# Performance work log

Measured on AMD Instinct MI355X. Metric: run time of the kernel, lower is better.

Reference implementation:

```python
import jax, jax.numpy as jnp
import numpy as np

N_NODES = 50000
N_EDGES = 800000
LN_EPS = 1e-5


def _segment_softmax_aggr(msg, t, dst, n):
    # SoftmaxAggregation(learn=True): alpha = softmax(msg * t) per dest segment, out = sum(alpha * msg)
    logits = msg * t  # [E, C]
    m = jax.ops.segment_max(logits, dst, num_segments=n)
    m = jnp.where(jnp.isfinite(m), m, 0.0)  # empty segments -> 0 to keep exp finite
    e = jnp.exp(logits - m[dst])
    denom = jax.ops.segment_sum(e, dst, num_segments=n)
    alpha = e / jnp.maximum(denom[dst], 1e-16)
    return jax.ops.segment_sum(alpha * msg, dst, num_segments=n)


def _sage_conv(x, src, dst, wp, bp, t, wl, bl, wr):
    # project=True: messages come from relu(lin(x)); root term uses ORIGINAL x
    xp = jax.nn.relu(x @ wp + bp)
    msg = xp[src]                                   # [E, C] gather
    aggr = _segment_softmax_aggr(msg, t, dst, x.shape[0])
    out = aggr @ wl + bl + x @ wr
    # normalize=True: L2 normalize rows (eps as in F.normalize)
    nrm = jnp.maximum(jnp.linalg.norm(out, axis=-1, keepdims=True), 1e-12)
    return out / nrm


def _mem_pool(x, k, w_conv, wl, bl):
    # PyG MemPooling, tau=1: Student-t kernel 1/(1+d^2)
    H, K, F = k.shape
    kk = k.reshape(H * K, F)
    d2 = (jnp.sum(kk * kk, -1)[:, None] + jnp.sum(x * x, -1)[None, :]
          - 2.0 * kk @ x.T)                          # [H*K, N]
    d2 = jnp.maximum(d2, 0.0)
    dist = 1.0 / (1.0 + d2)
    dist = dist.reshape(H, K, -1).transpose(0, 2, 1)  # [H, N, K]
    S = dist / jnp.sum(dist, -1, keepdims=True)       # per-head normalize over clusters
    S = jnp.einsum('h,hnk->nk', w_conv, S)            # 1x1 conv mixing heads (no bias)
    S = jax.nn.softmax(S, axis=-1)                    # [N, K]
    xp = S.T @ x                                      # [K, F]
    return xp @ wl + bl                               # [K, out]


def setup_inputs() -> dict:
    key = jax.random.key(0)
    ks = jax.random.split(key, 20)
    rn = lambda i, shp, s: jax.random.normal(ks[i], shp, dtype=jnp.float32) * s
    inp = {
        'x': rn(0, (N_NODES, 64), 1.0),
        'edge_index': jax.random.randint(ks[1], (2, N_EDGES), 0, N_NODES, dtype=jnp.int32),
        'w_proj1': rn(2, (64, 64), 0.1), 'b_proj1': rn(3, (64,), 0.05),
        't1': jnp.ones((64,), jnp.float32),
        'w_l1': rn(4, (64, 256), 0.1), 'b_l1': rn(5, (256,), 0.05),
        'w_r1': rn(6, (64, 256), 0.1),
        'w_proj2': rn(7, (256, 256), 0.05), 'b_proj2': rn(8, (256,), 0.05),
        't2': jnp.ones((256,), jnp.float32),
        'w_l2': rn(9, (256, 128), 0.05), 'b_l2': rn(10, (128,), 0.05),
        'w_r2': rn(11, (256, 128), 0.05),
        'k_mem': rn(12, (4, 4, 128), 1.0),
        'w_conv': rn(13, (4,), 0.5),
        'w_memlin': rn(14, (128, 128), 0.08), 'b_memlin': rn(15, (128,), 0.05),
        'w_fx': rn(16, (128, 64), 0.08), 'b_fx': rn(17, (64,), 0.05),
        'gamma': jnp.ones((64,), jnp.float32),
        'beta': jnp.zeros((64,), jnp.float32),
    }
    return inp


def reference(x, edge_index, w_proj1, b_proj1, t1, w_l1, b_l1, w_r1,
              w_proj2, b_proj2, t2, w_l2, b_l2, w_r2,
              k_mem, w_conv, w_memlin, b_memlin, w_fx, b_fx, gamma, beta):
    src, dst = edge_index[0], edge_index[1]
    h = _sage_conv(x, src, dst, w_proj1, b_proj1, t1, w_l1, b_l1, w_r1)
    h = jax.nn.relu(h)                              # dropout = identity (eval)
    h = _sage_conv(h, src, dst, w_proj2, b_proj2, t2, w_l2, b_l2, w_r2)
    h = jax.nn.relu(h)
    pooled = _mem_pool(h, k_mem, w_conv, w_memlin, b_memlin)  # [4, 128]
    g = jnp.mean(pooled, axis=0, keepdims=True)     # global_mean_pool -> [1, 128]
    y = g @ w_fx + b_fx                             # [1, 64]
    mu = jnp.mean(y, -1, keepdims=True)
    var = jnp.var(y, -1, keepdims=True)
    y = (y - mu) / jnp.sqrt(var + LN_EPS) * gamma + beta
    return jax.nn.relu(y)
```

## Files before the change

kernel.cpp:

```cpp
#include <hip/hip_runtime.h>
#include <hip/hip_bf16.h>

#define N_NODES 50000
#define N_EDGES 800000
#define NB 196
#define NBK 512
#define EPB 1563
#define PC_SLICES 2048
#define NWAVES 8192

typedef __attribute__((ext_vector_type(8))) short short8;
typedef __attribute__((ext_vector_type(4))) float f32x4;
typedef __attribute__((ext_vector_type(2))) float f32x2;

#define QSCALE2 (2.f / 255.f)
#define QINV2   127.5f
#define QSCALE1 (12.75f / 255.f)
#define QINV1   20.f

__device__ __forceinline__ float us2f(unsigned short u) {
    return __uint_as_float(((unsigned int)u) << 16);
}
__device__ __forceinline__ unsigned short f2bu(float f) {
    unsigned int u = __float_as_uint(f);
    unsigned int r = (u + 0x7fffu + ((u >> 16) & 1u)) >> 16;
    return (unsigned short)r;
}
__device__ __forceinline__ float exp2_hw(float x) {
    float r;
    __asm__("v_exp_f32 %0, %1" : "=v"(r) : "v"(x));
    return r;
}
__device__ __forceinline__ void async16(const void* g, void* l) {
    __builtin_amdgcn_global_load_lds(
        (const __attribute__((address_space(1))) unsigned int*)g,
        (__attribute__((address_space(3))) unsigned int*)l, 16, 0, 0);
}
#define LOG2E 1.44269504088896f

__global__ void k_hist(const int* __restrict__ dst, int* __restrict__ counts) {
    int e = blockIdx.x * 256 + threadIdx.x;
    if (e < N_EDGES) atomicAdd(&counts[dst[e]], 1);
}

__global__ __launch_bounds__(256) void k_scan1(const int* __restrict__ counts,
                                               int* __restrict__ row_ptr,
                                               int* __restrict__ partial) {
    __shared__ int sd[256];
    int t = threadIdx.x, i = blockIdx.x * 256 + t;
    int v = (i < N_NODES) ? counts[i] : 0;
    sd[t] = v;
    __syncthreads();
    for (int off = 1; off < 256; off <<= 1) {
        int o = (t >= off) ? sd[t - off] : 0;
        __syncthreads();
        sd[t] += o;
        __syncthreads();
    }
    if (i < N_NODES) row_ptr[i] = sd[t] - v;
    if (t == 255) partial[blockIdx.x] = sd[255];
}

__global__ __launch_bounds__(256) void k_scan3b(int* __restrict__ row_ptr,
                                                const int* __restrict__ partial) {
    __shared__ int sd[256];
    int t = threadIdx.x;
    sd[t] = (t < blockIdx.x) ? partial[t] : 0;
    __syncthreads();
    for (int off = 128; off > 0; off >>= 1) {
        if (t < off) sd[t] += sd[t + off];
        __syncthreads();
    }
    int base = sd[0];
    int i = blockIdx.x * 256 + t;
    if (i < N_NODES) row_ptr[i] += base;
    if (blockIdx.x == 0 && t == 0) row_ptr[N_NODES] = N_EDGES;
}

__global__ __launch_bounds__(256) void k_bhist(const int* __restrict__ dst,
                                               int* __restrict__ bcnt) {
    __shared__ int h[196];
    int t = threadIdx.x, b = blockIdx.x;
    if (t < 196) h[t] = 0;
    __syncthreads();
    int e0 = b * EPB, e1 = e0 + EPB < N_EDGES ? e0 + EPB : N_EDGES;
    for (int e = e0 + t; e < e1; e += 256) atomicAdd(&h[dst[e] >> 8], 1);
    __syncthreads();
    if (t < 196) bcnt[b * 196 + t] = h[t];
}

__global__ __launch_bounds__(512) void k_bscan(const int* __restrict__ bcnt,
                                               const int* __restrict__ row_ptr,
                                               int* __restrict__ boff) {
    __shared__ int sd[512];
    int q = blockIdx.x, t = threadIdx.x;
    int v = bcnt[t * 196 + q];
    sd[t] = v;
    __syncthreads();
    for (int off = 1; off < 512; off <<= 1) {
        int o = (t >= off) ? sd[t - off] : 0;
        __syncthreads();
        sd[t] += o;
        __syncthreads();
    }
    boff[t * 196 + q] = row_ptr[q * 256] + sd[t] - v;
}

__global__ __launch_bounds__(256) void k_bucket2(const int* __restrict__ src,
                                                 const int* __restrict__ dst,
                                                 const int* __restrict__ boff,
                                                 int* __restrict__ tmp) {
    __shared__ int lcur[196];
    int t = threadIdx.x, b = blockIdx.x;
    if (t < 196) lcur[t] = boff[b * 196 + t];
    __syncthreads();
    int e0 = b * EPB, e1 = e0 + EPB < N_EDGES ? e0 + EPB : N_EDGES;
    for (int e = e0 + t; e < e1; e += 256) {
        int d = dst[e];
        int pos = atomicAdd(&lcur[d >> 8], 1);
        tmp[pos] = src[e] | ((d & 255) << 16);
    }
}

__global__ __launch_bounds__(256) void k_scatter2(const int* __restrict__ row_ptr,
                                                  const int* __restrict__ tmp,
                                                  int* __restrict__ src_sorted) {
    __shared__ int lcur[256];
    int b = blockIdx.x, t = threadIdx.x;
    int n0 = b * 256;
    int nhi = n0 + 256 < N_NODES ? n0 + 256 : N_NODES;
    if (n0 + t < nhi) lcur[t] = row_ptr[n0 + t];
    __syncthreads();
    int ebeg = row_ptr[n0], eend = row_ptr[nhi];
    for (int i = ebeg + t; i < eend; i += 256) {
        int w = tmp[i];
        int pos = atomicAdd(&lcur[(w >> 16) & 255], 1);
        src_sorted[pos] = w & 0xFFFF;
    }
}

__global__ __launch_bounds__(256) void k_split(const int* __restrict__ row_ptr,
                                               int* __restrict__ split) {
    int w = blockIdx.x * 256 + threadIdx.x;
    if (w > NWAVES) return;
    if (w == NWAVES) { split[w] = N_NODES; return; }
    int target = (int)((long long)w * N_EDGES / NWAVES);
    int lo = 0, hi = N_NODES;
    while (lo < hi) {
        int mid = (lo + hi) >> 1;
        if (row_ptr[mid] < target) lo = mid + 1; else hi = mid;
    }
    split[w] = lo;
}

#define XCAST_N (N_NODES * 64)
#define PREP_TOT (XCAST_N + 167936)
__global__ __launch_bounds__(256) void k_prep(const float* __restrict__ x,
                                              const float* __restrict__ wp1,
                                              const float* __restrict__ wl1,
                                              const float* __restrict__ wr1,
                                              const float* __restrict__ wp2,
                                              const float* __restrict__ wl2,
                                              const float* __restrict__ wr2,
                                              unsigned short* __restrict__ cat1,
                                              unsigned short* __restrict__ B0T,
                                              unsigned short* __restrict__ B1T,
                                              unsigned short* __restrict__ BP2T,
                                              unsigned short* __restrict__ B2T) {
    int idx = (blockIdx.x * 256 + threadIdx.x) * 4;
    if (idx < XCAST_N) {
        int i = idx >> 6, j = idx & 63;
        float4 v = *(const float4*)&x[idx];
        ushort4 o = { f2bu(v.x), f2bu(v.y), f2bu(v.z), f2bu(v.w) };
        *(ushort4*)&cat1[i * 128 + 64 + j] = o;
        return;
    }
    int w = idx - XCAST_N;
    if (w < 4096)  { float4 v = *(const float4*)&wp1[w]; int k = w >> 6, n = w & 63;
                     B0T[n*64+k]=f2bu(v.x); B0T[(n+1)*64+k]=f2bu(v.y);
                     B0T[(n+2)*64+k]=f2bu(v.z); B0T[(n+3)*64+k]=f2bu(v.w); return; }
    w -= 4096;
    if (w < 16384) { float4 v = *(const float4*)&wl1[w]; int k = w >> 8, n = w & 255;
                     B1T[n*128+k]=f2bu(v.x); B1T[(n+1)*128+k]=f2bu(v.y);
                     B1T[(n+2)*128+k]=f2bu(v.z); B1T[(n+3)*128+k]=f2bu(v.w); return; }
    w -= 16384;
    if (w < 16384) { float4 v = *(const float4*)&wr1[w]; int k = w >> 8, n = w & 255;
                     B1T[n*128+64+k]=f2bu(v.x); B1T[(n+1)*128+64+k]=f2bu(v.y);
                     B1T[(n+2)*128+64+k]=f2bu(v.z); B1T[(n+3)*128+64+k]=f2bu(v.w); return; }
    w -= 16384;
    if (w < 65536) { float4 v = *(const float4*)&wp2[w]; int k = w >> 8, n = w & 255;
                     BP2T[n*256+k]=f2bu(v.x); BP2T[(n+1)*256+k]=f2bu(v.y);
                     BP2T[(n+2)*256+k]=f2bu(v.z); BP2T[(n+3)*256+k]=f2bu(v.w); return; }
    w -= 65536;
    if (w < 32768) { float4 v = *(const float4*)&wl2[w]; int k = w >> 7, n = w & 127;
                     B2T[n*512+k]=f2bu(v.x); B2T[(n+1)*512+k]=f2bu(v.y);
                     B2T[(n+2)*512+k]=f2bu(v.z); B2T[(n+3)*512+k]=f2bu(v.w); return; }
    w -= 32768;
    if (w < 32768) { float4 v = *(const float4*)&wr2[w]; int k = w >> 7, n = w & 127;
                     B2T[n*512+256+k]=f2bu(v.x); B2T[(n+1)*512+256+k]=f2bu(v.y);
                     B2T[(n+2)*512+256+k]=f2bu(v.z); B2T[(n+3)*512+256+k]=f2bu(v.w); return; }
}

template<int K, int C, int LDA, int LDOUT, int OUT_OFF, int EP, int WPB, int MH, int PIPE>
__global__ __launch_bounds__(256, WPB) void k_gemm(const unsigned short* __restrict__ A,
                                                   const unsigned short* __restrict__ BT,
                                                   const float* __restrict__ bias,
                                                   void* __restrict__ outv,
                                                   const float* __restrict__ kmem,
                                                   const float* __restrict__ wconv,
                                                   float* __restrict__ Sm,
                                                   float qinv) {
    constexpr int NT = C / 16;
    constexpr int SAE = 64 * MH * 64;
    constexpr int SBE = C * 64;
    constexpr int BUFE = SAE + SBE;
    constexpr int STAGE_B = BUFE * 2 * (PIPE ? 2 : 1);
    constexpr int RPLD = (EP == 2) ? (C + 4) : ((EP == 3) ? (C + 16) : (C + 8));
    constexpr int RP_B = 64 * RPLD * (EP == 2 ? 4 : (EP == 3 ? 1 : 2));
    constexpr int SMEM_B = STAGE_B > RP_B ? STAGE_B : RP_B;
    constexpr int POOL_B = (EP == 2) ? (2048 * 4 + 64 + 16) : 16;
    __shared__ __align__(16) char smem[SMEM_B + POOL_B];
    unsigned short* sA = (unsigned short*)smem;
    float* kls  = (float*)(smem + SMEM_B);
    float* kk2s = kls + 2048;
    float* wcs  = kk2s + 16;

    int t = threadIdx.x;
    int wid = t >> 6, lane = t & 63;
    int lrow = lane & 15, quad = lane >> 4;
    int m0 = blockIdx.x * (64 * MH);

    if (EP == 2) {
        for (int i = t; i < 2048; i += 256) kls[i] = kmem[i];
        if (t < 4) wcs[t] = wconv[t];
        __syncthreads();
        if (t < 16) {
            float s = 0.f;
            for (int f = 0; f < 128; ++f) { float v = kls[t * 128 + f]; s += v * v; }
            kk2s[t] = s;
        }
    }

    f32x4 acc[MH][NT];
#pragma unroll
    for (int h = 0; h < MH; ++h)
#pragma unroll
        for (int nt = 0; nt < NT; ++nt)
#pragma unroll
            for (int r = 0; r < 4; ++r) acc[h][nt][r] = 0.f;

    auto stage = [&](int step, int buf) {
        unsigned short* sAb = sA + buf * BUFE;
        unsigned short* sBb = sAb + SAE;
        int k0 = step * 64;
        for (int i = t; i < 64 * MH * 8; i += 256) {
            int r = i >> 3, seg = i & 7;
            size_t m = (size_t)(m0 + r);
            async16(&A[m * LDA + k0 + ((seg ^ (r & 7)) << 3)],
                    (char*)sAb + (size_t)(i - lane) * 16);
        }
        for (int i = t; i < C * 8; i += 256) {
            int n = i >> 3, seg = i & 7;
            async16(&BT[(size_t)n * K + k0 + ((seg ^ (n & 7)) << 3)],
                    (char*)sBb + (size_t)(i - lane) * 16);
        }
    };
    auto compute = [&](int buf) {
        unsigned short* sAb = sA + buf * BUFE;
        unsigned short* sBb = sAb + SAE;
#pragma unroll
        for (int kk = 0; kk < 2; ++kk) {
            int sw = lrow & 7;
            short8 av[MH];
#pragma unroll
            for (int h = 0; h < MH; ++h)
                av[h] = *(const short8*)&sAb[(h * 64 + wid * 16 + lrow) * 64 +
                                             (((kk * 4 + quad) ^ sw) << 3)];
#pragma unroll
            for (int nt = 0; nt < NT; ++nt) {
                short8 bfg = *(const short8*)&sBb[(nt * 16 + lrow) * 64 +
                                                  (((kk * 4 + quad) ^ sw) << 3)];
#pragma unroll
                for (int h = 0; h < MH; ++h)
                    acc[h][nt] = __builtin_amdgcn_mfma_f32_16x16x32_bf16(av[h], bfg, acc[h][nt], 0, 0, 0);
            }
        }
    };

    constexpr int NSTEP = K / 64;
    if (PIPE) {
        stage(0, 0);
        __syncthreads();
        for (int step = 0; step < NSTEP; ++step) {
            int cur = step & 1;
            if (step + 1 < NSTEP) stage(step + 1, cur ^ 1);
            compute(cur);
            __syncthreads();
        }
    } else {
        for (int step = 0; step < NSTEP; ++step) {
            __syncthreads();
            stage(step, 0);
            __syncthreads();
            compute(0);
        }
    }

#pragma unroll
    for (int h = 0; h < MH; ++h) {
#pragma unroll
        for (int nt = 0; nt < NT; ++nt) {
            float bv = bias[nt * 16 + lrow];
#pragma unroll
            for (int r = 0; r < 4; ++r) acc[h][nt][r] += bv;
        }
        if (EP == 1 || EP == 2) {
#pragma unroll
            for (int r = 0; r < 4; ++r) {
                float ss = 0.f;
#pragma unroll
                for (int nt = 0; nt < NT; ++nt) ss += acc[h][nt][r] * acc[h][nt][r];
                ss += __shfl_xor(ss, 1);
                ss += __shfl_xor(ss, 2);
                ss += __shfl_xor(ss, 4);
                ss += __shfl_xor(ss, 8);
                float rinv = 1.f / fmaxf(sqrtf(ss), 1e-12f);
#pragma unroll
                for (int nt = 0; nt < NT; ++nt)
                    acc[h][nt][r] = fmaxf(acc[h][nt][r] * rinv, 0.f);
            }
        } else {
#pragma unroll
            for (int nt = 0; nt < NT; ++nt)
#pragma unroll
                for (int r = 0; r < 4; ++r) acc[h][nt][r] = fmaxf(acc[h][nt][r], 0.f);
        }
    }

    __syncthreads();
#pragma unroll
    for (int h = 0; h < MH; ++h) {
        if (EP == 2) {
            float* rp = (float*)smem;
#pragma unroll
            for (int nt = 0; nt < NT; ++nt)
#pragma unroll
                for (int r = 0; r < 4; ++r)
                    rp[(wid * 16 + quad * 4 + r) * RPLD + nt * 16 + lrow] = acc[h][nt][r];
            __syncthreads();
            float* outp = (float*)outv;
            for (int i = t; i < 64 * C / 4; i += 256) {
                int f = i * 4, r = f / C, c = f % C;
                int m = m0 + h * 64 + r;
                if (m < N_NODES)
                    *(float4*)&outp[(size_t)m * LDOUT + OUT_OFF + c] = *(const float4*)&rp[r * RPLD + c];
            }
            {
                int row = t >> 2, p = t & 3;
                int cbase = p * 32;
                float dots[16];
#pragma unroll
                for (int k = 0; k < 16; ++k) dots[k] = 0.f;
                float x2 = 0.f;
#pragma unroll
                for (int j = 0; j < 8; ++j) {
                    int c4 = (j + p * 2) & 7;
                    float4 xv = *(const float4*)&rp[row * RPLD + cbase + c4 * 4];
                    x2 += xv.x * xv.x + xv.y * xv.y + xv.z * xv.z + xv.w * xv.w;
#pragma unroll
                    for (int k = 0; k < 16; ++k) {
                        float4 kv = *(const float4*)&kls[k * 128 + cbase + c4 * 4];
                        dots[k] += xv.x * kv.x + xv.y * kv.y + xv.z * kv.z + xv.w * kv.w;
                    }
                }
#pragma unroll
                for (int k = 0; k < 16; ++k) {
                    dots[k] += __shfl_xor(dots[k], 1);
                    dots[k] += __shfl_xor(dots[k], 2);
                }
                x2 += __shfl_xor(x2, 1);
                x2 += __shfl_xor(x2, 2);
                if (p == 0) {
                    int m = m0 + h * 64 + row;
                    if (m < N_NODES) {
                        float dist[16];
#pragma unroll
                        for (int k = 0; k < 16; ++k) {
                            float d2 = fmaxf(kk2s[k] + x2 - 2.f * dots[k], 0.f);
                            dist[k] = 1.f / (1.f + d2);
                        }
                        float s0 = 0.f, s1 = 0.f, s2 = 0.f, s3 = 0.f;
#pragma unroll
                        for (int hh = 0; hh < 4; ++hh) {
                            float den = dist[hh * 4] + dist[hh * 4 + 1] +
                                        dist[hh * 4 + 2] + dist[hh * 4 + 3];
                            float inv = wcs[hh] / den;
                            s0 += dist[hh * 4 + 0] * inv;
                            s1 += dist[hh * 4 + 1] * inv;
                            s2 += dist[hh * 4 + 2] * inv;
                            s3 += dist[hh * 4 + 3] * inv;
                        }
                        float mx = fmaxf(fmaxf(s0, s1), fmaxf(s2, s3));
                        float e0 = __expf(s0 - mx), e1 = __expf(s1 - mx);
                        float e2 = __expf(s2 - mx), e3 = __expf(s3 - mx);
                        float inv = 1.f / (e0 + e1 + e2 + e3);
                        *(float4*)&Sm[(size_t)m * 4] =
                            make_float4(e0 * inv, e1 * inv, e2 * inv, e3 * inv);
                    }
                }
            }
            __syncthreads();
        } else if (EP == 3) {
            unsigned char* rp = (unsigned char*)smem;
#pragma unroll
            for (int nt = 0; nt < NT; ++nt)
#pragma unroll
                for (int r = 0; r < 4; ++r) {
                    float q = fminf(__builtin_rintf(acc[h][nt][r] * qinv), 255.f);
                    rp[(wid * 16 + quad * 4 + r) * RPLD + nt * 16 + lrow] = (unsigned char)(int)q;
                }
            __syncthreads();
            unsigned char* outp = (unsigned char*)outv;
            for (int i = t; i < 64 * C / 16; i += 256) {
                int f = i * 16, r = f / C, c = f % C;
                int m = m0 + h * 64 + r;
                if (m < N_NODES)
                    *(uint4*)&outp[(size_t)m * LDOUT + OUT_OFF + c] = *(const uint4*)&rp[r * RPLD + c];
            }
            __syncthreads();
        } else {
            unsigned short* rp = (unsigned short*)smem;
#pragma unroll
            for (int nt = 0; nt < NT; ++nt)
#pragma unroll
                for (int r = 0; r < 4; ++r)
                    rp[(wid * 16 + quad * 4 + r) * RPLD + nt * 16 + lrow] = f2bu(acc[h][nt][r]);
            __syncthreads();
            unsigned short* outp = (unsigned short*)outv;
            for (int i = t; i < 64 * C / 8; i += 256) {
                int f = i * 8, r = f / C, c = f % C;
                int m = m0 + h * 64 + r;
                if (m < N_NODES)
                    *(uint4*)&outp[(size_t)m * LDOUT + OUT_OFF + c] = *(const uint4*)&rp[r * RPLD + c];
            }
            __syncthreads();
        }
    }
}

__global__ __launch_bounds__(256, 4) void k_aggr256(const unsigned char* __restrict__ xp,
                                                    const float* __restrict__ tvec,
                                                    const int* __restrict__ row_ptr,
                                                    const int* __restrict__ srcs,
                                                    const int* __restrict__ split,
                                                    unsigned short* __restrict__ outp) {
    int t = threadIdx.x & 63;
    int w = blockIdx.x * 4 + (threadIdx.x >> 6);
    float4 tv4 = *(const float4*)&tvec[t * 4];
    f32x2 tv01 = {tv4.x * (LOG2E * QSCALE2), tv4.y * (LOG2E * QSCALE2)};
    f32x2 tv23 = {tv4.z * (LOG2E * QSCALE2), tv4.w * (LOG2E * QSCALE2)};
    int n    = __builtin_amdgcn_readfirstlane(split[w]);
    int nend = __builtin_amdgcn_readfirstlane(split[w + 1]);
    if (n >= nend) return;
    int e    = __builtin_amdgcn_readfirstlane(row_ptr[n]);
    int eend = __builtin_amdgcn_readfirstlane(row_ptr[nend]);
    int rp_next = __builtin_amdgcn_readfirstlane(row_ptr[n + 1]);
    f32x2 se01 = {0.f, 0.f}, se23 = {0.f, 0.f};
    f32x2 sem01 = {0.f, 0.f}, sem23 = {0.f, 0.f};

#define FINALIZE()                                                             \
    {                                                                          \
        ushort4 o;                                                             \
        o.x = f2bu(QSCALE2 * sem01.x / fmaxf(se01.x, 1e-16f));                 \
        o.y = f2bu(QSCALE2 * sem01.y / fmaxf(se01.y, 1e-16f));                 \
        o.z = f2bu(QSCALE2 * sem23.x / fmaxf(se23.x, 1e-16f));                 \
        o.w = f2bu(QSCALE2 * sem23.y / fmaxf(se23.y, 1e-16f));                 \
        *(ushort4*)&outp[(size_t)n * 512 + t * 4] = o;                         \
        se01 = (f32x2){0.f, 0.f}; se23 = (f32x2){0.f, 0.f};                    \
        sem01 = (f32x2){0.f, 0.f}; sem23 = (f32x2){0.f, 0.f};                  \
        ++n;                                                                   \
        rp_next = (n < nend) ? __builtin_amdgcn_readfirstlane(row_ptr[n + 1])  \
                             : 0x7FFFFFFF;                                     \
    }
#define EDGE_BODY(VV)                                                          \
    {                                                                          \
        f32x2 m01 = {(float)((VV) & 0xFFu), (float)(((VV) >> 8) & 0xFFu)};     \
        f32x2 m23 = {(float)(((VV) >> 16) & 0xFFu), (float)((VV) >> 24)};      \
        f32x2 l01 = m01 * tv01, l23 = m23 * tv23;                              \
        f32x2 w01, w23;                                                        \
        w01.x = exp2_hw(l01.x); w01.y = exp2_hw(l01.y);                        \
        w23.x = exp2_hw(l23.x); w23.y = exp2_hw(l23.y);                        \
        se01 += w01; se23 += w23;                                              \
        sem01 = __builtin_elementwise_fma(w01, m01, sem01);                    \
        sem23 = __builtin_elementwise_fma(w23, m23, sem23);                    \
    }

    while (rp_next <= e) FINALIZE();

    while (e < eend) {
        unsigned int v[16];
        int rem = eend - e;
        int cnt = rem > 16 ? 16 : rem;
        if (cnt == 16) {
#pragma unroll
            for (int j = 0; j < 16; ++j) {
                const unsigned char* p = xp + (size_t)srcs[e + j] * 256;
                v[j] = *(const unsigned int*)&p[t * 4];
            }
        } else {
#pragma unroll
            for (int j = 0; j < 16; ++j) {
                int ee = e + j;
                ee = ee < eend ? ee : eend - 1;
                const unsigned char* p = xp + (size_t)srcs[ee] * 256;
                v[j] = *(const unsigned int*)&p[t * 4];
            }
        }
#pragma unroll
        for (int j = 0; j < 16; ++j) {
            if (j < cnt) {
                EDGE_BODY(v[j])
                while (e + j + 1 == rp_next) FINALIZE();
            }
        }
        e += cnt;
    }
#undef EDGE_BODY
#undef FINALIZE
}

__global__ __launch_bounds__(256, 4) void k_aggr64(const unsigned char* __restrict__ xp,
                                                   const float* __restrict__ tvec,
                                                   const int* __restrict__ row_ptr,
                                                   const int* __restrict__ srcs,
                                                   const int* __restrict__ split,
                                                   unsigned short* __restrict__ outp) {
    int c = threadIdx.x & 63;
    int w = blockIdx.x * 4 + (threadIdx.x >> 6);
    float tv = tvec[c] * (LOG2E * QSCALE1);
    int n    = __builtin_amdgcn_readfirstlane(split[w]);
    int nend = __builtin_amdgcn_readfirstlane(split[w + 1]);
    if (n >= nend) return;
    int e    = __builtin_amdgcn_readfirstlane(row_ptr[n]);
    int eend = __builtin_amdgcn_readfirstlane(row_ptr[nend]);
    int rp_next = __builtin_amdgcn_readfirstlane(row_ptr[n + 1]);
    float se = 0.f, sem = 0.f;

#define FIN1()                                                                 \
    {                                                                          \
        outp[(size_t)n * 128 + c] = f2bu(QSCALE1 * sem / fmaxf(se, 1e-16f));   \
        se = 0.f; sem = 0.f;                                                   \
        ++n;                                                                   \
        rp_next = (n < nend) ? __builtin_amdgcn_readfirstlane(row_ptr[n + 1])  \
                             : 0x7FFFFFFF;                                     \
    }

    while (rp_next <= e) FIN1();

    while (e < eend) {
        unsigned char v[16];
        int rem = eend - e;
        int cnt = rem > 16 ? 16 : rem;
        if (cnt == 16) {
#pragma unroll
            for (int j = 0; j < 16; ++j)
                v[j] = xp[(size_t)srcs[e + j] * 64 + c];
        } else {
#pragma unroll
            for (int j = 0; j < 16; ++j) {
                int ee = e + j;
                ee = ee < eend ? ee : eend - 1;
                v[j] = xp[(size_t)srcs[ee] * 64 + c];
            }
        }
#pragma unroll
        for (int j = 0; j < 16; ++j) {
            if (j < cnt) {
                float msg = (float)v[j];
                float wv = exp2_hw(msg * tv);
                se += wv;
                sem = fmaf(wv, msg, sem);
                while (e + j + 1 == rp_next) FIN1();
            }
        }
        e += cnt;
    }
#undef FIN1
}

__global__ __launch_bounds__(256) void k_pool_c(const float* __restrict__ h2,
                                                const float* __restrict__ Sm,
                                                float* __restrict__ part) {
    int t = threadIdx.x;
    int c = t & 127, sub = t >> 7;
    int slice = blockIdx.x * 2 + sub;
    float a0 = 0.f, a1 = 0.f, a2 = 0.f, a3 = 0.f;
    for (int n = slice; n < N_NODES; n += PC_SLICES) {
        float xv = h2[(size_t)n * 128 + c];
        float4 sv = *(const float4*)&Sm[(size_t)n * 4];
        a0 = fmaf(sv.x, xv, a0);
        a1 = fmaf(sv.y, xv, a1);
        a2 = fmaf(sv.z, xv, a2);
        a3 = fmaf(sv.w, xv, a3);
    }
    float* p = &part[(size_t)slice * 512];
    p[0 * 128 + c] = a0;
    p[1 * 128 + c] = a1;
    p[2 * 128 + c] = a2;
    p[3 * 128 + c] = a3;
}

__global__ __launch_bounds__(256) void k_pool_b(const float* __restrict__ part,
                                                float* __restrict__ pooled) {
    int j = blockIdx.x;
    float s = 0.f;
    for (int b = threadIdx.x; b < PC_SLICES; b += 256) s += part[(size_t)b * 512 + j];
#pragma unroll
    for (int off = 32; off > 0; off >>= 1) s += __shfl_xor(s, off);
    __shared__ float red[4];
    int lane = threadIdx.x & 63, wid = threadIdx.x >> 6;
    if (lane == 0) red[wid] = s;
    __syncthreads();
    if (threadIdx.x == 0) pooled[j] = red[0] + red[1] + red[2] + red[3];
}

__global__ __launch_bounds__(128) void k_final(const float* __restrict__ pooled,
                                               const float* __restrict__ wmem,
                                               const float* __restrict__ bmem,
                                               const float* __restrict__ wfx,
                                               const float* __restrict__ bfx,
                                               const float* __restrict__ gamma,
                                               const float* __restrict__ beta,
                                               float* __restrict__ out) {
    __shared__ float gx[128], g[128];
    int t = threadIdx.x;
    gx[t] = 0.25f * (pooled[t] + pooled[128 + t] + pooled[256 + t] + pooled[384 + t]);
    __syncthreads();
    float acc = bmem[t];
    for (int f = 0; f < 128; ++f) acc = fmaf(gx[f], wmem[f * 128 + t], acc);
    g[t] = acc;
    __syncthreads();
    if (t < 64) {
        float y = bfx[t];
        for (int f = 0; f < 128; ++f) y = fmaf(g[f], wfx[f * 64 + t], y);
        float s = y, s2 = y * y;
#pragma unroll
        for (int off = 32; off > 0; off >>= 1) {
            s += __shfl_xor(s, off);
            s2 += __shfl_xor(s2, off);
        }
        float mu = s * (1.f / 64.f);
        float var = s2 * (1.f / 64.f) - mu * mu;
        float v = (y - mu) / sqrtf(var + 1e-5f) * gamma[t] + beta[t];
        out[t] = fmaxf(v, 0.f);
    }
}

extern "C" void kernel_launch(void* const* d_in, const int* in_sizes, int n_in,
                              void* d_out, int out_size, void* d_ws, size_t ws_size,
                              hipStream_t stream) {
    const float* x        = (const float*)d_in[0];
    const int*   ei       = (const int*)  d_in[1];
    const float* w_proj1  = (const float*)d_in[2];
    const float* b_proj1  = (const float*)d_in[3];
    const float* t1       = (const float*)d_in[4];
    const float* w_l1     = (const float*)d_in[5];
    const float* b_l1     = (const float*)d_in[6];
    const float* w_r1     = (const float*)d_in[7];
    const float* w_proj2  = (const float*)d_in[8];
    const float* b_proj2  = (const float*)d_in[9];
    const float* t2       = (const float*)d_in[10];
    const float* w_l2     = (const float*)d_in[11];
    const float* b_l2     = (const float*)d_in[12];
    const float* w_r2     = (const float*)d_in[13];
    const float* k_mem    = (const float*)d_in[14];
    const float* w_conv   = (const float*)d_in[15];
    const float* w_memlin = (const float*)d_in[16];
    const float* b_memlin = (const float*)d_in[17];
    const float* w_fx     = (const float*)d_in[18];
    const float* b_fx     = (const float*)d_in[19];
    const float* gamma    = (const float*)d_in[20];
    const float* beta     = (const float*)d_in[21];
    const int* src = ei;
    const int* dst = ei + N_EDGES;
    (void)in_sizes; (void)n_in; (void)out_size; (void)ws_size;

    char* W = (char*)d_ws;
    const size_t MB = 1024 * 1024;
    int*   row_ptr    = (int*)(W + 0);
    int*   counts     = (int*)(W + 256 * 1024);
    int*   partial    = (int*)(W + 512 * 1024);
    int*   split      = (int*)(W + 520 * 1024);
    int*   src_sorted = (int*)(W + 768 * 1024);
    unsigned short* cat1 = (unsigned short*)(W + 4 * MB);
    unsigned char*  xp1  = (unsigned char*)(W + 17 * MB);
    unsigned short* cat2 = (unsigned short*)(W + 24 * MB);
    unsigned char*  xp2  = (unsigned char*)(W + 76 * MB);
    float* h2     = (float*)(W + 102 * MB);
    float* Sm     = (float*)(W + 128 * MB);
    float* pooled = (float*)(W + 131 * MB);
    unsigned short* B0T  = (unsigned short*)(W + 133 * MB);
    unsigned short* B1T  = (unsigned short*)(W + 134 * MB);
    unsigned short* BP2T = (unsigned short*)(W + 135 * MB);
    unsigned short* B2T  = (unsigned short*)(W + 136 * MB);
    int*   boff   = (int*)(W + 137 * MB);
    int*   bcnt   = (int*)(W + 138 * MB);
    float* part   = (float*)(W + 140 * MB);
    int*   tmp_e  = (int*)(W + 144 * MB);

    hipMemsetAsync(counts, 0, N_NODES * sizeof(int), stream);
    k_hist<<<(N_EDGES + 255) / 256, 256, 0, stream>>>(dst, counts);
    k_bhist<<<NBK, 256, 0, stream>>>(dst, bcnt);
    k_scan1<<<NB, 256, 0, stream>>>(counts, row_ptr, partial);
    k_scan3b<<<NB, 256, 0, stream>>>(row_ptr, partial);
    k_bscan<<<NB, 512, 0, stream>>>(bcnt, row_ptr, boff);
    k_split<<<(NWAVES + 1 + 255) / 256, 256, 0, stream>>>(row_ptr, split);
    k_bucket2<<<NBK, 256, 0, stream>>>(src, dst, boff, tmp_e);
    k_scatter2<<<NB, 256, 0, stream>>>(row_ptr, tmp_e, src_sorted);

    k_prep<<<(PREP_TOT / 4 + 255) / 256, 256, 0, stream>>>(
        x, w_proj1, w_l1, w_r1, w_proj2, w_l2, w_r2, cat1, B0T, B1T, BP2T, B2T);

    const int GB = (N_NODES + 127) / 128;
    const int AGB = NWAVES / 4;

    k_gemm<64, 64, 128, 64, 0, 3, 4, 2, 0><<<GB, 256, 0, stream>>>(
        cat1 + 64, B0T, b_proj1, xp1, nullptr, nullptr, nullptr, QINV1);
    k_aggr64<<<AGB, 256, 0, stream>>>(xp1, t1, row_ptr, src_sorted, split, cat1);
    k_gemm<128, 256, 128, 512, 256, 1, 3, 2, 0><<<GB, 256, 0, stream>>>(
        cat1, B1T, b_l1, cat2, nullptr, nullptr, nullptr, 0.f);

    k_gemm<256, 256, 512, 256, 0, 3, 3, 2, 0><<<GB, 256, 0, stream>>>(
        cat2 + 256, BP2T, b_proj2, xp2, nullptr, nullptr, nullptr, QINV2);
    k_aggr256<<<AGB, 256, 0, stream>>>(xp2, t2, row_ptr, src_sorted, split, cat2);
    k_gemm<512, 128, 512, 128, 0, 2, 3, 2, 1><<<GB, 256, 0, stream>>>(
        cat2, B2T, b_l2, h2, k_mem, w_conv, Sm, 0.f);

    k_pool_c<<<PC_SLICES / 2, 256, 0, stream>>>(h2, Sm, part);
    k_pool_b<<<512, 256, 0, stream>>>(part, pooled);
    k_final<<<1, 128, 0, stream>>>(pooled, w_memlin, b_memlin, w_fx, b_fx, gamma, beta,
                                   (float*)d_out);
}
```

Before: 346.5 us.

## Split 256-channel aggregation into four 64-channel slices per wave

Reworks the second-layer softmax aggregation so each block handles one 64-channel slice of the 256-byte quantized row, with each lane processing one byte instead of four. Each wave loops over four edge-range partitions spaced 2048 apart, and the grid is fixed at 2048 blocks. The aim is more parallel gathers and less per-lane arithmetic and register pressure. In exchange, each gathered source index is now loaded four times (once per slice), and the per-lane gathers and stores become byte- and short-sized, which are less efficient.

```diff
diff --git a/kernel.cpp b/kernel.cpp
--- a/kernel.cpp
+++ b/kernel.cpp
@@ -454,79 +454,66 @@
                                                     const int* __restrict__ srcs,
                                                     const int* __restrict__ split,
                                                     unsigned short* __restrict__ outp) {
-    int t = threadIdx.x & 63;
-    int w = blockIdx.x * 4 + (threadIdx.x >> 6);
-    float4 tv4 = *(const float4*)&tvec[t * 4];
-    f32x2 tv01 = {tv4.x * (LOG2E * QSCALE2), tv4.y * (LOG2E * QSCALE2)};
-    f32x2 tv23 = {tv4.z * (LOG2E * QSCALE2), tv4.w * (LOG2E * QSCALE2)};
-    int n    = __builtin_amdgcn_readfirstlane(split[w]);
-    int nend = __builtin_amdgcn_readfirstlane(split[w + 1]);
-    if (n >= nend) return;
-    int e    = __builtin_amdgcn_readfirstlane(row_ptr[n]);
-    int eend = __builtin_amdgcn_readfirstlane(row_ptr[nend]);
-    int rp_next = __builtin_amdgcn_readfirstlane(row_ptr[n + 1]);
-    f32x2 se01 = {0.f, 0.f}, se23 = {0.f, 0.f};
-    f32x2 sem01 = {0.f, 0.f}, sem23 = {0.f, 0.f};
-
-#define FINALIZE()                                                             \
+    int lane = threadIdx.x & 63;
+    int wid  = threadIdx.x >> 6;
+    int b = blockIdx.x;
+    int slice = b & 3;
+    int base = (b >> 2) * 4 + wid;
+    float tv = tvec[slice * 64 + lane] * (LOG2E * QSCALE2);
+    const unsigned char* xps = xp + slice * 64;
+    unsigned short* outs = outp + slice * 64;
+
+#define FINS()                                                                 \
     {                                                                          \
-        ushort4 o;                                                             \
-        o.x = f2bu(QSCALE2 * sem01.x / fmaxf(se01.x, 1e-16f));                 \
-        o.y = f2bu(QSCALE2 * sem01.y / fmaxf(se01.y, 1e-16f));                 \
-        o.z = f2bu(QSCALE2 * sem23.x / fmaxf(se23.x, 1e-16f));                 \
-        o.w = f2bu(QSCALE2 * sem23.y / fmaxf(se23.y, 1e-16f));                 \
-        *(ushort4*)&outp[(size_t)n * 512 + t * 4] = o;                         \
-        se01 = (f32x2){0.f, 0.f}; se23 = (f32x2){0.f, 0.f};                    \
-        sem01 = (f32x2){0.f, 0.f}; sem23 = (f32x2){0.f, 0.f};                  \
+        outs[(size_t)n * 512 + lane] = f2bu(QSCALE2 * sem / fmaxf(se, 1e-16f));\
+        se = 0.f; sem = 0.f;                                                   \
         ++n;                                                                   \
         rp_next = (n < nend) ? __builtin_amdgcn_readfirstlane(row_ptr[n + 1])  \
                              : 0x7FFFFFFF;                                     \
     }
-#define EDGE_BODY(VV)                                                          \
-    {                                                                          \
-        f32x2 m01 = {(float)((VV) & 0xFFu), (float)(((VV) >> 8) & 0xFFu)};     \
-        f32x2 m23 = {(float)(((VV) >> 16) & 0xFFu), (float)((VV) >> 24)};      \
-        f32x2 l01 = m01 * tv01, l23 = m23 * tv23;                              \
-        f32x2 w01, w23;                                                        \
-        w01.x = exp2_hw(l01.x); w01.y = exp2_hw(l01.y);                        \
-        w23.x = exp2_hw(l23.x); w23.y = exp2_hw(l23.y);                        \
-        se01 += w01; se23 += w23;                                              \
-        sem01 = __builtin_elementwise_fma(w01, m01, sem01);                    \
-        sem23 = __builtin_elementwise_fma(w23, m23, sem23);                    \
-    }
-
-    while (rp_next <= e) FINALIZE();
-
-    while (e < eend) {
-        unsigned int v[16];
-        int rem = eend - e;
-        int cnt = rem > 16 ? 16 : rem;
-        if (cnt == 16) {
+
+    for (int k = 0; k < 4; ++k) {
+        int w = base + k * 2048;
+        int n    = __builtin_amdgcn_readfirstlane(split[w]);
+        int nend = __builtin_amdgcn_readfirstlane(split[w + 1]);
+        if (n >= nend) continue;
+        int e    = __builtin_amdgcn_readfirstlane(row_ptr[n]);
+        int eend = __builtin_amdgcn_readfirstlane(row_ptr[nend]);
+        int rp_next = __builtin_amdgcn_readfirstlane(row_ptr[n + 1]);
+        float se = 0.f, sem = 0.f;
+
+        while (rp_next <= e) FINS();
+
+        while (e < eend) {
+            unsigned char v[16];
+            int rem = eend - e;
+            int cnt = rem > 16 ? 16 : rem;
+            if (cnt == 16) {
+#pragma unroll
+                for (int j = 0; j < 16; ++j)
+                    v[j] = xps[(size_t)srcs[e + j] * 256 + lane];
+            } else {
+#pragma unroll
+                for (int j = 0; j < 16; ++j) {
+                    int ee = e + j;
+                    ee = ee < eend ? ee : eend - 1;
+                    v[j] = xps[(size_t)srcs[ee] * 256 + lane];
+                }
+            }
 #pragma unroll
             for (int j = 0; j < 16; ++j) {
-                const unsigned char* p = xp + (size_t)srcs[e + j] * 256;
-                v[j] = *(const unsigned int*)&p[t * 4];
-            }
-        } else {
-#pragma unroll
-            for (int j = 0; j < 16; ++j) {
-                int ee = e + j;
-                ee = ee < eend ? ee : eend - 1;
-                const unsigned char* p = xp + (size_t)srcs[ee] * 256;
-                v[j] = *(const unsigned int*)&p[t * 4];
-            }
-        }
-#pragma unroll
-        for (int j = 0; j < 16; ++j) {
-            if (j < cnt) {
-                EDGE_BODY(v[j])
-                while (e + j + 1 == rp_next) FINALIZE();
-            }
-        }
-        e += cnt;
-    }
-#undef EDGE_BODY
-#undef FINALIZE
+                if (j < cnt) {
+                    float msg = (float)v[j];
+                    float wv = exp2_hw(msg * tv);
+                    se += wv;
+                    sem = fmaf(wv, msg, sem);
+                    while (e + j + 1 == rp_next) FINS();
+                }
+            }
+            e += cnt;
+        }
+    }
+#undef FINS
 }
 
 __global__ __launch_bounds__(256, 4) void k_aggr64(const unsigned char* __restrict__ xp,
@@ -732,7 +719,7 @@
 
     k_gemm<256, 256, 512, 256, 0, 3, 3, 2, 0><<<GB, 256, 0, stream>>>(
         cat2 + 256, BP2T, b_proj2, xp2, nullptr, nullptr, nullptr, QINV2);
-    k_aggr256<<<AGB, 256, 0, stream>>>(xp2, t2, row_ptr, src_sorted, split, cat2);
+    k_aggr256<<<2048, 256, 0, stream>>>(xp2, t2, row_ptr, src_sorted, split, cat2);
     k_gemm<512, 128, 512, 128, 0, 2, 3, 2, 1><<<GB, 256, 0, stream>>>(
         cat2, B2T, b_l2, h2, k_mem, w_conv, Sm, 0.f);
 
```

Result: slower. 393.1 us (+13.5%).
